# Kernel tuning notes

Measured on AMD Instinct MI355X. Metric: run time of the kernel, lower is better.

## Reference

```python
import jax, jax.numpy as jnp
import numpy as np

H = 16          # num_heads
EPS = 1e-6      # RMSNorm eps


def _rms_norm(t, w):
    # t: [..., head_dim], w: [head_dim]
    var = jnp.mean(jnp.square(t), axis=-1, keepdims=True)
    return t * jax.lax.rsqrt(var + EPS) * w


def setup_inputs() -> dict:
    key = jax.random.key(0)
    ks = jax.random.split(key, 8)
    B, N, M, C = 2, 2048, 256, 1024
    s = 0.02
    return {
        "x": jax.random.normal(ks[0], (B, N, C), jnp.float32),
        "y": jax.random.normal(ks[1], (B, M, C), jnp.float32),
        "qkv_w": jax.random.normal(ks[2], (3 * C, C), jnp.float32) * s,
        "qkv_b": jax.random.normal(ks[3], (3 * C,), jnp.float32) * s,
        "kv_w": jax.random.normal(ks[4], (2 * C, C), jnp.float32) * s,
        "kv_b": jax.random.normal(ks[5], (2 * C,), jnp.float32) * s,
        "qn_w": jnp.ones((C // H,), jnp.float32),
        "kn_w": jnp.ones((C // H,), jnp.float32),
        "proj_w": jax.random.normal(ks[6], (C, C), jnp.float32) * s,
        "proj_b": jax.random.normal(ks[7], (C,), jnp.float32) * s,
    }


def reference(x, y, qkv_w, qkv_b, kv_w, kv_b, qn_w, kn_w, proj_w, proj_b):
    B, N, C = x.shape
    M = y.shape[1]
    hd = C // H
    scale = hd ** -0.5

    # fused QKV projection for image tokens -> [B, H, N, hd] each
    qkv = (jnp.einsum('bnc,oc->bno', x, qkv_w) + qkv_b).reshape(B, N, 3, H, hd)
    qkv = jnp.transpose(qkv, (2, 0, 3, 1, 4))
    q, kx, vx = qkv[0], qkv[1], qkv[2]

    # qk-norm (RMSNorm over head_dim)
    q = _rms_norm(q, qn_w)
    kx = _rms_norm(kx, kn_w)

    # KV projection for text tokens -> [B, H, M, hd] each
    kvy = (jnp.einsum('bmc,oc->bmo', y, kv_w) + kv_b).reshape(B, M, 2, H, hd)
    kvy = jnp.transpose(kvy, (2, 0, 3, 1, 4))
    ky, vy = kvy[0], kvy[1]
    ky = _rms_norm(ky, kn_w)

    # concat image+text KV along the sequence axis
    k = jnp.concatenate([kx, ky], axis=2)  # [B, H, N+M, hd]
    v = jnp.concatenate([vx, vy], axis=2)

    # scaled dot-product attention
    logits = jnp.einsum('bhnd,bhsd->bhns', q, k) * scale  # [B, H, N, N+M]
    attn = jax.nn.softmax(logits, axis=-1)
    out = jnp.einsum('bhns,bhsd->bhnd', attn, v)          # [B, H, N, hd]

    out = jnp.transpose(out, (0, 2, 1, 3)).reshape(B, N, C)
    return jnp.einsum('bnc,oc->bno', out, proj_w) + proj_b
```

## Files before the change

### kernel.cpp

```cpp
#include <hip/hip_runtime.h>

#define BATCH 2
#define NTOK 2048
#define MTOK 256
#define CDIM 1024
#define NHEAD 16
#define HD 64
#define SEQ (NTOK + MTOK)
#define TOK_X (BATCH * NTOK)
#define TOK_Y (BATCH * MTOK)
#define BHN (BATCH * NHEAD)
#define NKT (SEQ / 64)

typedef __attribute__((ext_vector_type(8))) short bf16x8;
typedef __attribute__((ext_vector_type(4))) short bf16x4;
typedef __attribute__((ext_vector_type(4))) float f32x4;
typedef __attribute__((ext_vector_type(2))) unsigned int u32x2;
#if __has_builtin(__builtin_amdgcn_cvt_pk_bf16_f32)
typedef __attribute__((ext_vector_type(2))) __bf16 bf16x2_t;
#endif

__device__ __forceinline__ float b2f(ushort u) {
    unsigned v = ((unsigned)u) << 16;
    return __builtin_bit_cast(float, v);
}
__device__ __forceinline__ ushort f2b(float f) {
    unsigned u = __builtin_bit_cast(unsigned, f);
    u += 0x7fffu + ((u >> 16) & 1u);
    return (ushort)(u >> 16);
}
__device__ __forceinline__ unsigned pack2bf(float a, float b) {
#if __has_builtin(__builtin_amdgcn_cvt_pk_bf16_f32)
    bf16x2_t h = __builtin_amdgcn_cvt_pk_bf16_f32(a, b);
    return __builtin_bit_cast(unsigned, h);
#else
    return ((unsigned)f2b(b) << 16) | (unsigned)f2b(a);
#endif
}

__device__ __forceinline__ void async_load16(const ushort* g, ushort* l) {
    __builtin_amdgcn_global_load_lds(
        (const __attribute__((address_space(1))) unsigned*)(const void*)g,
        (__attribute__((address_space(3))) unsigned*)(void*)l, 16, 0, 0);
}

__global__ __launch_bounds__(256) void cast_all(
    const float* __restrict__ s0, ushort* __restrict__ t0, int b0,
    const float* __restrict__ s1, ushort* __restrict__ t1, int b1,
    const float* __restrict__ s2, ushort* __restrict__ t2, int b2,
    const float* __restrict__ s3, ushort* __restrict__ t3, int b3,
    const float* __restrict__ s4, ushort* __restrict__ t4) {
    int blk = blockIdx.x;
    const float* s; ushort* t;
    if (blk < b0)      { s = s0; t = t0; }
    else if (blk < b1) { s = s1; t = t1; blk -= b0; }
    else if (blk < b2) { s = s2; t = t2; blk -= b1; }
    else if (blk < b3) { s = s3; t = t3; blk -= b2; }
    else               { s = s4; t = t4; blk -= b3; }
    int i = (blk * 256 + threadIdx.x) * 8;
    float4 a = *(const float4*)(s + i);
    float4 b = *(const float4*)(s + i + 4);
    ushort tmp[8] = {f2b(a.x), f2b(a.y), f2b(a.z), f2b(a.w),
                     f2b(b.x), f2b(b.y), f2b(b.z), f2b(b.w)};
    *(uint4*)(t + i) = *(const uint4*)tmp;
}

template <int MODE>
__global__ __launch_bounds__(256) void gemm_fused(const ushort* __restrict__ A,
                                                  const ushort* __restrict__ Bt,
                                                  const float* __restrict__ bias,
                                                  float* __restrict__ Cf,
                                                  ushort* __restrict__ d_q,
                                                  ushort* __restrict__ d_k,
                                                  ushort* __restrict__ d_v,
                                                  const float* __restrict__ qn_w,
                                                  const float* __restrict__ kn_w,
                                                  int M, int N, int K) {
    __shared__ ushort As[128][64];
    __shared__ ushort Bs[128][64];
    int tid = threadIdx.x;
    int lane = tid & 63;
    int w = tid >> 6;
    int wm = (w >> 1) * 64;
    int wn = (w & 1) * 64;
    int l15 = lane & 15;
    int quad = lane >> 4;
    int sw = l15 & 7;
    int bm = blockIdx.y * 128;
    int bn = blockIdx.x * 128;

    f32x4 acc[4][4];
#pragma unroll
    for (int i = 0; i < 4; i++)
#pragma unroll
        for (int j = 0; j < 4; j++) acc[i][j] = (f32x4)0.0f;

    int lrow = lane >> 3;
    int lcol = ((lane & 7) ^ lrow) * 8;

    for (int k0 = 0; k0 < K; k0 += 64) {
        __syncthreads();
#pragma unroll
        for (int p = 0; p < 4; p++) {
            int rb = w * 32 + p * 8;
            async_load16(&A[(size_t)(bm + rb + lrow) * K + k0 + lcol], &As[rb][0]);
            async_load16(&Bt[(size_t)(bn + rb + lrow) * K + k0 + lcol], &Bs[rb][0]);
        }
        __syncthreads();
#pragma unroll
        for (int kk = 0; kk < 64; kk += 32) {
            bf16x8 af[4], bfr[4];
            int g = (kk >> 3) + quad;
            int csw = (g ^ sw) * 8;
#pragma unroll
            for (int i = 0; i < 4; i++)
                af[i] = *(const bf16x8*)&As[wm + i * 16 + l15][csw];
#pragma unroll
            for (int j = 0; j < 4; j++)
                bfr[j] = *(const bf16x8*)&Bs[wn + j * 16 + l15][csw];
#pragma unroll
            for (int i = 0; i < 4; i++)
#pragma unroll
                for (int j = 0; j < 4; j++)
                    acc[i][j] = __builtin_amdgcn_mfma_f32_16x16x32_bf16(af[i], bfr[j], acc[i][j], 0, 0, 0);
        }
    }

    int colbase = bn + wn;
    float bv[4];
#pragma unroll
    for (int j = 0; j < 4; j++) bv[j] = bias[colbase + j * 16 + l15];
#pragma unroll
    for (int i = 0; i < 4; i++)
#pragma unroll
        for (int j = 0; j < 4; j++)
#pragma unroll
            for (int r = 0; r < 4; r++) acc[i][j][r] += bv[j];

    if (MODE == 0) {
#pragma unroll
        for (int i = 0; i < 4; i++) {
            int row0 = bm + wm + i * 16 + quad * 4;
#pragma unroll
            for (int j = 0; j < 4; j++) {
                int col = colbase + j * 16 + l15;
#pragma unroll
                for (int r = 0; r < 4; r++)
                    Cf[(size_t)(row0 + r) * N + col] = acc[i][j][r];
            }
        }
        return;
    }

    int region = colbase >> 10;
    int h = (colbase >> 6) & (NHEAD - 1);
    bool do_norm = (MODE == 1) ? (region <= 1) : (region == 0);
    if (do_norm) {
        const float* wv = (MODE == 1 && region == 0) ? qn_w : kn_w;
        float wj[4];
#pragma unroll
        for (int j = 0; j < 4; j++) wj[j] = wv[j * 16 + l15];
        float qs = (MODE == 1 && region == 0) ? (0.125f * 1.44269504088896f) : 1.0f;
#pragma unroll
        for (int i = 0; i < 4; i++)
#pragma unroll
            for (int r = 0; r < 4; r++) {
                float s = acc[i][0][r] * acc[i][0][r] + acc[i][1][r] * acc[i][1][r]
                        + acc[i][2][r] * acc[i][2][r] + acc[i][3][r] * acc[i][3][r];
                s += __shfl_xor(s, 1);
                s += __shfl_xor(s, 2);
                s += __shfl_xor(s, 4);
                s += __shfl_xor(s, 8);
                float rs = rsqrtf(s * (1.0f / 64.0f) + 1e-6f) * qs;
#pragma unroll
                for (int j = 0; j < 4; j++) acc[i][j][r] *= rs * wj[j];
            }
    }
#pragma unroll
    for (int i = 0; i < 4; i++) {
#pragma unroll
        for (int r = 0; r < 4; r++) {
            int t = bm + wm + i * 16 + quad * 4 + r;
            size_t base;
            ushort* dst;
            if (MODE == 1) {
                int b = t >> 11, n = t & (NTOK - 1);
                size_t bh = (size_t)(b * NHEAD + h);
                if (region == 0)      { dst = d_q; base = (bh * NTOK + n) * 64; }
                else if (region == 1) { dst = d_k; base = (bh * SEQ + n) * 64; }
                else                  { dst = d_v; base = (bh * SEQ + n) * 64; }
            } else {
                int b = t >> 8, m = t & (MTOK - 1);
                size_t bh = (size_t)(b * NHEAD + h);
                if (region == 0) { dst = d_k; base = (bh * SEQ + NTOK + m) * 64; }
                else             { dst = d_v; base = (bh * SEQ + NTOK + m) * 64; }
            }
#pragma unroll
            for (int j = 0; j < 4; j++)
                dst[base + j * 16 + l15] = f2b(acc[i][j][r]);
        }
    }
}

__global__ __launch_bounds__(256) void transpose_v(const ushort* __restrict__ vc,
                                                   ushort* __restrict__ vt) {
    __shared__ ushort t[64][72];
    int bh = blockIdx.y;
    int s0 = blockIdx.x * 64;
    int tid = threadIdx.x;
    int r = tid >> 3, c = (tid & 7) * 8;
    const ushort* src = vc + ((size_t)bh * SEQ + s0) * 64;
    *(uint4*)&t[r][c] = *(const uint4*)&src[(size_t)r * 64 + c];
    *(uint4*)&t[r + 32][c] = *(const uint4*)&src[(size_t)(r + 32) * 64 + c];
    __syncthreads();
    ushort* dst = vt + (size_t)bh * 64 * SEQ + s0;
#pragma unroll
    for (int p = 0; p < 2; p++) {
        int d = (tid >> 3) + p * 32;
        int s8 = (tid & 7) * 8;
        ushort tmp[8];
#pragma unroll
        for (int i = 0; i < 8; i++) tmp[i] = t[s8 + i][d];
        *(uint4*)&dst[(size_t)d * SEQ + s8] = *(const uint4*)tmp;
    }
}

__global__ __launch_bounds__(256) void attn_fwd(const ushort* __restrict__ qh,
                                                const ushort* __restrict__ kc,
                                                const ushort* __restrict__ vt,
                                                ushort* __restrict__ out) {
    __shared__ ushort Ks[2][64][72];
    __shared__ ushort Vs[2][64][68];
    int tid = threadIdx.x;
    int lane = tid & 63;
    int w = tid >> 6;
    int l15 = lane & 15;
    int quad = lane >> 4;
    int bh = blockIdx.y;
    int q0 = blockIdx.x * 128 + w * 32;

    const ushort* qpA = qh + ((size_t)bh * NTOK + q0 + l15) * 64 + quad * 8;
    const ushort* qpB = qpA + 16 * 64;
    bf16x8 qA0 = *(const bf16x8*)qpA;
    bf16x8 qA1 = *(const bf16x8*)(qpA + 32);
    bf16x8 qB0 = *(const bf16x8*)qpB;
    bf16x8 qB1 = *(const bf16x8*)(qpB + 32);

    float lA = 0.0f, lB = 0.0f;
    f32x4 OA[4], OB[4];
#pragma unroll
    for (int jd = 0; jd < 4; jd++) { OA[jd] = (f32x4)0.0f; OB[jd] = (f32x4)0.0f; }

    const ushort* kbase = kc + (size_t)bh * SEQ * 64;
    const ushort* vbase = vt + (size_t)bh * 64 * SEQ;
    int sr = tid >> 3, sc = (tid & 7) * 8;
    const ushort* kp0 = kbase + (size_t)sr * 64 + sc;
    const ushort* kp1 = kbase + (size_t)(sr + 32) * 64 + sc;
    const ushort* vp0 = vbase + (size_t)sr * SEQ + sc;
    const ushort* vp1 = vbase + (size_t)(sr + 32) * SEQ + sc;

    uint4 rka = *(const uint4*)kp0;
    uint4 rkb = *(const uint4*)kp1;
    uint4 rva = *(const uint4*)vp0;
    uint4 rvb = *(const uint4*)vp1;

    for (int t = 0; t < NKT; t++) {
        int p = t & 1;
        *(uint4*)&Ks[p][sr][sc] = rka;
        *(uint4*)&Ks[p][sr + 32][sc] = rkb;
        *(uint4*)&Vs[p][sr][sc] = rva;
        *(uint4*)&Vs[p][sr + 32][sc] = rvb;
        __syncthreads();
        if (t + 1 < NKT) {
            int s0 = (t + 1) * 64;
            rka = *(const uint4*)(kp0 + (size_t)s0 * 64);
            rkb = *(const uint4*)(kp1 + (size_t)s0 * 64);
            rva = *(const uint4*)(vp0 + s0);
            rvb = *(const uint4*)(vp1 + s0);
        }

        f32x4 SA[4], SB[4];
#pragma unroll
        for (int j = 0; j < 4; j++) { SA[j] = (f32x4)0.0f; SB[j] = (f32x4)0.0f; }
#pragma unroll
        for (int j = 0; j < 4; j++) {
            bf16x8 kf = *(const bf16x8*)&Ks[p][j * 16 + l15][quad * 8];
            SA[j] = __builtin_amdgcn_mfma_f32_16x16x32_bf16(kf, qA0, SA[j], 0, 0, 0);
            SB[j] = __builtin_amdgcn_mfma_f32_16x16x32_bf16(kf, qB0, SB[j], 0, 0, 0);
        }
#pragma unroll
        for (int j = 0; j < 4; j++) {
            bf16x8 kf = *(const bf16x8*)&Ks[p][j * 16 + l15][32 + quad * 8];
            SA[j] = __builtin_amdgcn_mfma_f32_16x16x32_bf16(kf, qA1, SA[j], 0, 0, 0);
            SB[j] = __builtin_amdgcn_mfma_f32_16x16x32_bf16(kf, qB1, SB[j], 0, 0, 0);
        }

#pragma unroll
        for (int j = 0; j < 4; j++) {
            float a0 = __builtin_amdgcn_exp2f(SA[j][0]);
            float a1 = __builtin_amdgcn_exp2f(SA[j][1]);
            float a2 = __builtin_amdgcn_exp2f(SA[j][2]);
            float a3 = __builtin_amdgcn_exp2f(SA[j][3]);
            lA += (a0 + a1) + (a2 + a3);
            float b0 = __builtin_amdgcn_exp2f(SB[j][0]);
            float b1 = __builtin_amdgcn_exp2f(SB[j][1]);
            float b2 = __builtin_amdgcn_exp2f(SB[j][2]);
            float b3 = __builtin_amdgcn_exp2f(SB[j][3]);
            lB += (b0 + b1) + (b2 + b3);
            u32x2 pa, pb2;
            pa.x = pack2bf(a0, a1); pa.y = pack2bf(a2, a3);
            pb2.x = pack2bf(b0, b1); pb2.y = pack2bf(b2, b3);
            bf16x4 pbA = __builtin_bit_cast(bf16x4, pa);
            bf16x4 pbB = __builtin_bit_cast(bf16x4, pb2);
#pragma unroll
            for (int jd = 0; jd < 4; jd++) {
                bf16x4 vf = *(const bf16x4*)&Vs[p][jd * 16 + l15][j * 16 + quad * 4];
                OA[jd] = __builtin_amdgcn_mfma_f32_16x16x16bf16_1k(vf, pbA, OA[jd], 0, 0, 0);
                OB[jd] = __builtin_amdgcn_mfma_f32_16x16x16bf16_1k(vf, pbB, OB[jd], 0, 0, 0);
            }
        }
    }
    lA += __shfl_xor(lA, 16);
    lA += __shfl_xor(lA, 32);
    lB += __shfl_xor(lB, 16);
    lB += __shfl_xor(lB, 32);
    float invA = 1.0f / lA;
    float invB = 1.0f / lB;
    int b = bh >> 4, h = bh & 15;
    int tokA = (b << 11) + q0 + l15;
    ushort* obaseA = out + ((size_t)tokA * NHEAD + h) * 64;
    ushort* obaseB = obaseA + (size_t)16 * NHEAD * 64;
#pragma unroll
    for (int jd = 0; jd < 4; jd++) {
        u32x2 pk;
        pk.x = pack2bf(OA[jd][0] * invA, OA[jd][1] * invA);
        pk.y = pack2bf(OA[jd][2] * invA, OA[jd][3] * invA);
        *(u32x2*)&obaseA[jd * 16 + quad * 4] = pk;
        pk.x = pack2bf(OB[jd][0] * invB, OB[jd][1] * invB);
        pk.y = pack2bf(OB[jd][2] * invB, OB[jd][3] * invB);
        *(u32x2*)&obaseB[jd * 16 + quad * 4] = pk;
    }
}

extern "C" void kernel_launch(void* const* d_in, const int* in_sizes, int n_in,
                              void* d_out, int out_size, void* d_ws, size_t ws_size,
                              hipStream_t stream) {
    const float* x      = (const float*)d_in[0];
    const float* y      = (const float*)d_in[1];
    const float* qkv_w  = (const float*)d_in[2];
    const float* qkv_b  = (const float*)d_in[3];
    const float* kv_w   = (const float*)d_in[4];
    const float* kv_b   = (const float*)d_in[5];
    const float* qn_w   = (const float*)d_in[6];
    const float* kn_w   = (const float*)d_in[7];
    const float* proj_w = (const float*)d_in[8];
    const float* proj_b = (const float*)d_in[9];
    float* outp = (float*)d_out;

    char* ws = (char*)d_ws;
    ushort* x_bf    = (ushort*)ws; ws += (size_t)TOK_X * CDIM * 2;
    ushort* y_bf    = (ushort*)ws; ws += (size_t)TOK_Y * CDIM * 2;
    ushort* qkvw_bf = (ushort*)ws; ws += (size_t)3 * CDIM * CDIM * 2;
    ushort* kvw_bf  = (ushort*)ws; ws += (size_t)2 * CDIM * CDIM * 2;
    ushort* projw_bf= (ushort*)ws; ws += (size_t)CDIM * CDIM * 2;
    ushort* qh      = (ushort*)ws; ws += (size_t)BHN * NTOK * 64 * 2;
    ushort* kc      = (ushort*)ws; ws += (size_t)BHN * SEQ * 64 * 2;
    ushort* vc      = (ushort*)ws; ws += (size_t)BHN * SEQ * 64 * 2;
    ushort* vt      = (ushort*)ws; ws += (size_t)BHN * SEQ * 64 * 2;
    ushort* ao      = (ushort*)ws; ws += (size_t)TOK_X * CDIM * 2;

    int c0 = TOK_X * CDIM / 2048;
    int c1 = c0 + TOK_Y * CDIM / 2048;
    int c2 = c1 + 3 * CDIM * CDIM / 2048;
    int c3 = c2 + 2 * CDIM * CDIM / 2048;
    int c4 = c3 + CDIM * CDIM / 2048;
    cast_all<<<c4, 256, 0, stream>>>(x, x_bf, c0, y, y_bf, c1, qkv_w, qkvw_bf, c2,
                                     kv_w, kvw_bf, c3, proj_w, projw_bf);

    gemm_fused<1><<<dim3(3 * CDIM / 128, TOK_X / 128), 256, 0, stream>>>(
        x_bf, qkvw_bf, qkv_b, nullptr, qh, kc, vc, qn_w, kn_w, TOK_X, 3 * CDIM, CDIM);
    gemm_fused<2><<<dim3(2 * CDIM / 128, TOK_Y / 128), 256, 0, stream>>>(
        y_bf, kvw_bf, kv_b, nullptr, nullptr, kc, vc, qn_w, kn_w, TOK_Y, 2 * CDIM, CDIM);

    transpose_v<<<dim3(SEQ / 64, BHN), 256, 0, stream>>>(vc, vt);

    attn_fwd<<<dim3(NTOK / 128, BHN), 256, 0, stream>>>(qh, kc, vt, ao);

    gemm_fused<0><<<dim3(CDIM / 128, TOK_X / 128), 256, 0, stream>>>(
        ao, projw_bf, proj_b, outp, nullptr, nullptr, nullptr, nullptr, nullptr,
        TOK_X, CDIM, CDIM);
}
```

Measured before the change: 253.2 us.

## Use 128-key tiles and 16x16x32 MFMA for PV with permuted V layout

```diff
diff --git a/kernel.cpp b/kernel.cpp
--- a/kernel.cpp
+++ b/kernel.cpp
@@ -10,12 +10,13 @@
 #define TOK_X (BATCH * NTOK)
 #define TOK_Y (BATCH * MTOK)
 #define BHN (BATCH * NHEAD)
-#define NKT (SEQ / 64)
+#define NKT2 (SEQ / 128)
 
 typedef __attribute__((ext_vector_type(8))) short bf16x8;
 typedef __attribute__((ext_vector_type(4))) short bf16x4;
 typedef __attribute__((ext_vector_type(4))) float f32x4;
 typedef __attribute__((ext_vector_type(2))) unsigned int u32x2;
+typedef __attribute__((ext_vector_type(4))) unsigned int u32x4;
 #if __has_builtin(__builtin_amdgcn_cvt_pk_bf16_f32)
 typedef __attribute__((ext_vector_type(2))) __bf16 bf16x2_t;
 #endif
@@ -220,7 +221,11 @@
         int s8 = (tid & 7) * 8;
         ushort tmp[8];
 #pragma unroll
-        for (int i = 0; i < 8; i++) tmp[i] = t[s8 + i][d];
+        for (int i = 0; i < 8; i++) {
+            int cc = s8 + i;
+            int srcs = (cc & 32) + ((cc & 31) >> 1) + ((cc & 1) << 4);
+            tmp[i] = t[srcs][d];
+        }
         *(uint4*)&dst[(size_t)d * SEQ + s8] = *(const uint4*)tmp;
     }
 }
@@ -229,8 +234,8 @@
                                                 const ushort* __restrict__ kc,
                                                 const ushort* __restrict__ vt,
                                                 ushort* __restrict__ out) {
-    __shared__ ushort Ks[2][64][72];
-    __shared__ ushort Vs[2][64][68];
+    __shared__ ushort Ks[2][128][72];
+    __shared__ ushort Vs[2][64][136];
     int tid = threadIdx.x;
     int lane = tid & 63;
     int w = tid >> 6;
@@ -254,69 +259,71 @@
     const ushort* kbase = kc + (size_t)bh * SEQ * 64;
     const ushort* vbase = vt + (size_t)bh * 64 * SEQ;
     int sr = tid >> 3, sc = (tid & 7) * 8;
-    const ushort* kp0 = kbase + (size_t)sr * 64 + sc;
-    const ushort* kp1 = kbase + (size_t)(sr + 32) * 64 + sc;
-    const ushort* vp0 = vbase + (size_t)sr * SEQ + sc;
-    const ushort* vp1 = vbase + (size_t)(sr + 32) * SEQ + sc;
-
-    uint4 rka = *(const uint4*)kp0;
-    uint4 rkb = *(const uint4*)kp1;
-    uint4 rva = *(const uint4*)vp0;
-    uint4 rvb = *(const uint4*)vp1;
-
-    for (int t = 0; t < NKT; t++) {
-        int p = t & 1;
-        *(uint4*)&Ks[p][sr][sc] = rka;
-        *(uint4*)&Ks[p][sr + 32][sc] = rkb;
-        *(uint4*)&Vs[p][sr][sc] = rva;
-        *(uint4*)&Vs[p][sr + 32][sc] = rvb;
+    int vr = tid >> 4, vcl = (tid & 15) * 8;
+
+    uint4 rk[4], rv[4];
+#pragma unroll
+    for (int p = 0; p < 4; p++)
+        rk[p] = *(const uint4*)(kbase + (size_t)(sr + p * 32) * 64 + sc);
+#pragma unroll
+    for (int p = 0; p < 4; p++)
+        rv[p] = *(const uint4*)(vbase + (size_t)(vr + p * 16) * SEQ + vcl);
+
+    for (int t = 0; t < NKT2; t++) {
+        int pb_ = t & 1;
+#pragma unroll
+        for (int p = 0; p < 4; p++) *(uint4*)&Ks[pb_][sr + p * 32][sc] = rk[p];
+#pragma unroll
+        for (int p = 0; p < 4; p++) *(uint4*)&Vs[pb_][vr + p * 16][vcl] = rv[p];
         __syncthreads();
-        if (t + 1 < NKT) {
-            int s0 = (t + 1) * 64;
-            rka = *(const uint4*)(kp0 + (size_t)s0 * 64);
-            rkb = *(const uint4*)(kp1 + (size_t)s0 * 64);
-            rva = *(const uint4*)(vp0 + s0);
-            rvb = *(const uint4*)(vp1 + s0);
-        }
-
-        f32x4 SA[4], SB[4];
-#pragma unroll
-        for (int j = 0; j < 4; j++) { SA[j] = (f32x4)0.0f; SB[j] = (f32x4)0.0f; }
-#pragma unroll
-        for (int j = 0; j < 4; j++) {
-            bf16x8 kf = *(const bf16x8*)&Ks[p][j * 16 + l15][quad * 8];
+        if (t + 1 < NKT2) {
+            int s0 = (t + 1) * 128;
+#pragma unroll
+            for (int p = 0; p < 4; p++)
+                rk[p] = *(const uint4*)(kbase + (size_t)(s0 + sr + p * 32) * 64 + sc);
+#pragma unroll
+            for (int p = 0; p < 4; p++)
+                rv[p] = *(const uint4*)(vbase + (size_t)(vr + p * 16) * SEQ + s0 + vcl);
+        }
+
+        f32x4 SA[8], SB[8];
+#pragma unroll
+        for (int j = 0; j < 8; j++) { SA[j] = (f32x4)0.0f; SB[j] = (f32x4)0.0f; }
+#pragma unroll
+        for (int j = 0; j < 8; j++) {
+            bf16x8 kf = *(const bf16x8*)&Ks[pb_][j * 16 + l15][quad * 8];
             SA[j] = __builtin_amdgcn_mfma_f32_16x16x32_bf16(kf, qA0, SA[j], 0, 0, 0);
             SB[j] = __builtin_amdgcn_mfma_f32_16x16x32_bf16(kf, qB0, SB[j], 0, 0, 0);
         }
 #pragma unroll
-        for (int j = 0; j < 4; j++) {
-            bf16x8 kf = *(const bf16x8*)&Ks[p][j * 16 + l15][32 + quad * 8];
+        for (int j = 0; j < 8; j++) {
+            bf16x8 kf = *(const bf16x8*)&Ks[pb_][j * 16 + l15][32 + quad * 8];
             SA[j] = __builtin_amdgcn_mfma_f32_16x16x32_bf16(kf, qA1, SA[j], 0, 0, 0);
             SB[j] = __builtin_amdgcn_mfma_f32_16x16x32_bf16(kf, qB1, SB[j], 0, 0, 0);
         }
 
 #pragma unroll
-        for (int j = 0; j < 4; j++) {
-            float a0 = __builtin_amdgcn_exp2f(SA[j][0]);
-            float a1 = __builtin_amdgcn_exp2f(SA[j][1]);
-            float a2 = __builtin_amdgcn_exp2f(SA[j][2]);
-            float a3 = __builtin_amdgcn_exp2f(SA[j][3]);
-            lA += (a0 + a1) + (a2 + a3);
-            float b0 = __builtin_amdgcn_exp2f(SB[j][0]);
-            float b1 = __builtin_amdgcn_exp2f(SB[j][1]);
-            float b2 = __builtin_amdgcn_exp2f(SB[j][2]);
-            float b3 = __builtin_amdgcn_exp2f(SB[j][3]);
-            lB += (b0 + b1) + (b2 + b3);
-            u32x2 pa, pb2;
-            pa.x = pack2bf(a0, a1); pa.y = pack2bf(a2, a3);
-            pb2.x = pack2bf(b0, b1); pb2.y = pack2bf(b2, b3);
-            bf16x4 pbA = __builtin_bit_cast(bf16x4, pa);
-            bf16x4 pbB = __builtin_bit_cast(bf16x4, pb2);
+        for (int pb2 = 0; pb2 < 4; pb2++) {
+            int j0 = 2 * pb2, j1 = j0 + 1;
+            u32x4 wa, wb;
+#pragma unroll
+            for (int r = 0; r < 4; r++) {
+                float a0 = __builtin_amdgcn_exp2f(SA[j0][r]);
+                float a1 = __builtin_amdgcn_exp2f(SA[j1][r]);
+                lA += a0 + a1;
+                wa[r] = pack2bf(a0, a1);
+                float b0 = __builtin_amdgcn_exp2f(SB[j0][r]);
+                float b1 = __builtin_amdgcn_exp2f(SB[j1][r]);
+                lB += b0 + b1;
+                wb[r] = pack2bf(b0, b1);
+            }
+            bf16x8 pA = __builtin_bit_cast(bf16x8, wa);
+            bf16x8 pB = __builtin_bit_cast(bf16x8, wb);
 #pragma unroll
             for (int jd = 0; jd < 4; jd++) {
-                bf16x4 vf = *(const bf16x4*)&Vs[p][jd * 16 + l15][j * 16 + quad * 4];
-                OA[jd] = __builtin_amdgcn_mfma_f32_16x16x16bf16_1k(vf, pbA, OA[jd], 0, 0, 0);
-                OB[jd] = __builtin_amdgcn_mfma_f32_16x16x16bf16_1k(vf, pbB, OB[jd], 0, 0, 0);
+                bf16x8 vf = *(const bf16x8*)&Vs[pb_][jd * 16 + l15][pb2 * 32 + quad * 8];
+                OA[jd] = __builtin_amdgcn_mfma_f32_16x16x32_bf16(vf, pA, OA[jd], 0, 0, 0);
+                OB[jd] = __builtin_amdgcn_mfma_f32_16x16x32_bf16(vf, pB, OB[jd], 0, 0, 0);
             }
         }
     }
```

New measurement: 295.1 us. 16.5% more time.

## Use 16x16x32 bf16 MFMA for PV product with permuted V layout

Applied to the files above, without the earlier changes.

```diff
diff --git a/kernel.cpp b/kernel.cpp
--- a/kernel.cpp
+++ b/kernel.cpp
@@ -16,6 +16,7 @@
 typedef __attribute__((ext_vector_type(4))) short bf16x4;
 typedef __attribute__((ext_vector_type(4))) float f32x4;
 typedef __attribute__((ext_vector_type(2))) unsigned int u32x2;
+typedef __attribute__((ext_vector_type(4))) unsigned int u32x4;
 #if __has_builtin(__builtin_amdgcn_cvt_pk_bf16_f32)
 typedef __attribute__((ext_vector_type(2))) __bf16 bf16x2_t;
 #endif
@@ -220,7 +221,11 @@
         int s8 = (tid & 7) * 8;
         ushort tmp[8];
 #pragma unroll
-        for (int i = 0; i < 8; i++) tmp[i] = t[s8 + i][d];
+        for (int i = 0; i < 8; i++) {
+            int cc = s8 + i;
+            int srcs = (cc & 32) + ((cc & 31) >> 1) + ((cc & 1) << 4);
+            tmp[i] = t[srcs][d];
+        }
         *(uint4*)&dst[(size_t)d * SEQ + s8] = *(const uint4*)tmp;
     }
 }
@@ -296,27 +301,27 @@
         }
 
 #pragma unroll
-        for (int j = 0; j < 4; j++) {
-            float a0 = __builtin_amdgcn_exp2f(SA[j][0]);
-            float a1 = __builtin_amdgcn_exp2f(SA[j][1]);
-            float a2 = __builtin_amdgcn_exp2f(SA[j][2]);
-            float a3 = __builtin_amdgcn_exp2f(SA[j][3]);
-            lA += (a0 + a1) + (a2 + a3);
-            float b0 = __builtin_amdgcn_exp2f(SB[j][0]);
-            float b1 = __builtin_amdgcn_exp2f(SB[j][1]);
-            float b2 = __builtin_amdgcn_exp2f(SB[j][2]);
-            float b3 = __builtin_amdgcn_exp2f(SB[j][3]);
-            lB += (b0 + b1) + (b2 + b3);
-            u32x2 pa, pb2;
-            pa.x = pack2bf(a0, a1); pa.y = pack2bf(a2, a3);
-            pb2.x = pack2bf(b0, b1); pb2.y = pack2bf(b2, b3);
-            bf16x4 pbA = __builtin_bit_cast(bf16x4, pa);
-            bf16x4 pbB = __builtin_bit_cast(bf16x4, pb2);
+        for (int pb2 = 0; pb2 < 2; pb2++) {
+            int j0 = 2 * pb2, j1 = j0 + 1;
+            u32x4 wa, wb;
+#pragma unroll
+            for (int r = 0; r < 4; r++) {
+                float a0 = __builtin_amdgcn_exp2f(SA[j0][r]);
+                float a1 = __builtin_amdgcn_exp2f(SA[j1][r]);
+                lA += a0 + a1;
+                wa[r] = pack2bf(a0, a1);
+                float b0 = __builtin_amdgcn_exp2f(SB[j0][r]);
+                float b1 = __builtin_amdgcn_exp2f(SB[j1][r]);
+                lB += b0 + b1;
+                wb[r] = pack2bf(b0, b1);
+            }
+            bf16x8 pA = __builtin_bit_cast(bf16x8, wa);
+            bf16x8 pB = __builtin_bit_cast(bf16x8, wb);
 #pragma unroll
             for (int jd = 0; jd < 4; jd++) {
-                bf16x4 vf = *(const bf16x4*)&Vs[p][jd * 16 + l15][j * 16 + quad * 4];
-                OA[jd] = __builtin_amdgcn_mfma_f32_16x16x16bf16_1k(vf, pbA, OA[jd], 0, 0, 0);
-                OB[jd] = __builtin_amdgcn_mfma_f32_16x16x16bf16_1k(vf, pbB, OB[jd], 0, 0, 0);
+                bf16x8 vf = *(const bf16x8*)&Vs[p][jd * 16 + l15][pb2 * 32 + quad * 8];
+                OA[jd] = __builtin_amdgcn_mfma_f32_16x16x32_bf16(vf, pA, OA[jd], 0, 0, 0);
+                OB[jd] = __builtin_amdgcn_mfma_f32_16x16x32_bf16(vf, pB, OB[jd], 0, 0, 0);
             }
         }
     }
```

After: 252.9 us. No clear change (-0.1%).
